# Performance work log

Hardware: AMD Instinct MI355X
Metric: run time of the kernel (lower is better)

## Reference

```python
import jax, jax.numpy as jnp
import numpy as np

TEMPERATURE = 0.1
WEIGHT = 0.1
EPS = 1e-12  # F.normalize clamp_min eps

B = 512   # number of reactions (batches)
G = 128   # atoms per reaction per side (uniform groups)
D = 256   # feature dim


def setup_inputs() -> dict:
    key = jax.random.key(0)
    k1, k2, k3, k4 = jax.random.split(key, 4)
    preds = jax.random.normal(k1, (B,), dtype=jnp.float32)
    y = jax.random.normal(k2, (B,), dtype=jnp.float32)
    reactant_features = jax.random.normal(k3, (B * G, D), dtype=jnp.float32)
    product_features = jax.random.normal(k4, (B * G, D), dtype=jnp.float32)
    # sorted, uniform-size groups: [0]*G, [1]*G, ...
    batch_idx = jnp.repeat(jnp.arange(B, dtype=jnp.int64), G)
    return {
        "preds": preds,
        "y": y,
        "reactant_features": reactant_features,
        "product_features": product_features,
        "reactant_batch_indices": batch_idx,
        "product_batch_indices": batch_idx,
    }


def _l2_normalize(x):
    # matches F.normalize(p=2, dim=1): x / max(||x||, eps)
    n = jnp.sqrt(jnp.sum(x * x, axis=-1, keepdims=True))
    return x / jnp.maximum(n, EPS)


def reference(preds, y, reactant_features, product_features,
              reactant_batch_indices, product_batch_indices):
    # MSE with reduction='sum'
    mse_loss = jnp.sum((preds - y) ** 2)

    # groups are uniform and sorted -> per-batch gather == reshape
    nb = int(reactant_batch_indices[-1]) + 1          # number of unique batches
    g = reactant_features.shape[0] // nb
    d = reactant_features.shape[1]
    r = reactant_features.reshape(nb, g, d)
    p = product_features.reshape(nb, g, d)

    rn = _l2_normalize(r)
    pn = _l2_normalize(p)
    # per-batch similarity [nb, g, g]
    sim = jnp.einsum('bgd,bhd->bgh', rn, pn) / TEMPERATURE

    # cross_entropy with labels = arange(g), mean over rows (torch default)
    lse = jax.scipy.special.logsumexp(sim, axis=-1)   # [nb, g]
    diag = jnp.einsum('bgg->bg', sim)                 # logits at true labels
    ce_per_batch = jnp.mean(lse - diag, axis=-1)      # [nb]
    contrastive_loss = jnp.mean(ce_per_batch)         # sum over batches / nb

    return mse_loss + WEIGHT * contrastive_loss
```

## Files before the change

kernel.cpp:

```cpp
#include <hip/hip_runtime.h>
#include <hip/hip_bf16.h>
#include <math.h>

#define BATCH 512
#define G 128
#define D 256
#define LRP 264

typedef __attribute__((ext_vector_type(8))) short short8;
typedef __attribute__((ext_vector_type(4))) float f32x4;
typedef __attribute__((ext_vector_type(4))) int  i32x4;

__device__ __forceinline__ unsigned short bfbits(float x) {
    __hip_bfloat16 h = __float2bfloat16(x);
    union { __hip_bfloat16 h; unsigned short u; } c; c.h = h; return c.u;
}
__device__ __forceinline__ unsigned int pack2bf16(float a, float b) {
    return (unsigned int)bfbits(a) | ((unsigned int)bfbits(b) << 16);
}

__global__ __launch_bounds__(512, 4)
void fused_kernel(const float* __restrict__ rfeat,
                  const float* __restrict__ pfeat,
                  const float* __restrict__ preds,
                  const float* __restrict__ yv,
                  float* __restrict__ out)
{
    const int b = blockIdx.x;
    const float* rb = rfeat + (size_t)b * (G * D);
    const float* pb = pfeat + (size_t)b * (G * D);

    __shared__ unsigned short ps[64 * LRP];
    __shared__ float inv_r[G];
    __shared__ float inv_p[G];
    __shared__ float red[8];

    const int tid  = threadIdx.x;
    const int lane = tid & 63;
    const int wv   = tid >> 6;
    const int lg   = lane >> 4;
    const int lc   = lane & 15;

    const int srow = tid >> 4;
    const int sc4  = tid & 15;

    float contrib = 0.f;
    if (b == 0) {
        float dd = preds[tid] - yv[tid];
        contrib = dd * dd;
    }

    short8 afr[8];
    float nrsum = 0.f;
    const float* rptr = rb + (wv * 16 + lc) * D + lg * 8;
#pragma unroll
    for (int ks = 0; ks < 8; ++ks) {
        float4 x0 = *reinterpret_cast<const float4*>(rptr + ks * 32);
        float4 x1 = *reinterpret_cast<const float4*>(rptr + ks * 32 + 4);
        nrsum += x0.x*x0.x + x0.y*x0.y + x0.z*x0.z + x0.w*x0.w
               + x1.x*x1.x + x1.y*x1.y + x1.z*x1.z + x1.w*x1.w;
        i32x4 pk = { (int)pack2bf16(x0.x, x0.y), (int)pack2bf16(x0.z, x0.w),
                     (int)pack2bf16(x1.x, x1.y), (int)pack2bf16(x1.z, x1.w) };
        union { i32x4 i; short8 s; } u; u.i = pk;
        afr[ks] = u.s;
    }
    nrsum += __shfl_xor(nrsum, 16);
    nrsum += __shfl_xor(nrsum, 32);
    if (lane < 16)
        inv_r[wv * 16 + lane] = 10.0f / fmaxf(sqrtf(nrsum), 1e-12f);

    float4 pv[2][4];
#pragma unroll
    for (int it = 0; it < 2; ++it)
#pragma unroll
        for (int j = 0; j < 4; ++j)
            pv[it][j] = *reinterpret_cast<const float4*>(pb + (srow + 32 * it) * D + (sc4 + 16 * j) * 4);
#pragma unroll
    for (int it = 0; it < 2; ++it) {
        const int row = srow + 32 * it;
        float s = 0.f;
#pragma unroll
        for (int j = 0; j < 4; ++j) {
            const float4 v = pv[it][j];
            s += v.x*v.x + v.y*v.y + v.z*v.z + v.w*v.w;
            *reinterpret_cast<uint2*>(&ps[row * LRP + (sc4 + 16 * j) * 4]) =
                make_uint2(pack2bf16(v.x, v.y), pack2bf16(v.z, v.w));
        }
#pragma unroll
        for (int off = 1; off < 16; off <<= 1) s += __shfl_xor(s, off);
        if (sc4 == 0) inv_p[row] = 1.0f / fmaxf(sqrtf(s), 1e-12f);
    }
    __syncthreads();

    float4 qv[2][4];
#pragma unroll
    for (int it = 0; it < 2; ++it)
#pragma unroll
        for (int j = 0; j < 4; ++j)
            qv[it][j] = *reinterpret_cast<const float4*>(pb + (64 + srow + 32 * it) * D + (sc4 + 16 * j) * 4);

    f32x4 acc[8];
#pragma unroll
    for (int nj = 0; nj < 8; ++nj) acc[nj] = (f32x4){0.f, 0.f, 0.f, 0.f};

#pragma unroll
    for (int ks = 0; ks < 8; ++ks) {
        const int kb = ks * 32 + lg * 8;
#pragma unroll
        for (int nj = 0; nj < 4; ++nj) {
            short8 bfr = *reinterpret_cast<const short8*>(&ps[(nj * 16 + lc) * LRP + kb]);
            acc[nj] = __builtin_amdgcn_mfma_f32_16x16x32_bf16(afr[ks], bfr, acc[nj], 0, 0, 0);
        }
    }
    __syncthreads();

#pragma unroll
    for (int it = 0; it < 2; ++it) {
        const int row = srow + 32 * it;
        float s = 0.f;
#pragma unroll
        for (int j = 0; j < 4; ++j) {
            const float4 v = qv[it][j];
            s += v.x*v.x + v.y*v.y + v.z*v.z + v.w*v.w;
            *reinterpret_cast<uint2*>(&ps[row * LRP + (sc4 + 16 * j) * 4]) =
                make_uint2(pack2bf16(v.x, v.y), pack2bf16(v.z, v.w));
        }
#pragma unroll
        for (int off = 1; off < 16; off <<= 1) s += __shfl_xor(s, off);
        if (sc4 == 0) inv_p[64 + row] = 1.0f / fmaxf(sqrtf(s), 1e-12f);
    }
    __syncthreads();

#pragma unroll
    for (int ks = 0; ks < 8; ++ks) {
        const int kb = ks * 32 + lg * 8;
#pragma unroll
        for (int nj = 0; nj < 4; ++nj) {
            short8 bfr = *reinterpret_cast<const short8*>(&ps[(nj * 16 + lc) * LRP + kb]);
            acc[4 + nj] = __builtin_amdgcn_mfma_f32_16x16x32_bf16(afr[ks], bfr, acc[4 + nj], 0, 0, 0);
        }
    }

    float invp_r[8];
#pragma unroll
    for (int nj = 0; nj < 8; ++nj) invp_r[nj] = inv_p[nj * 16 + lc];

    const int njd = wv;
    float ce_part = 0.f;
#pragma unroll
    for (int reg = 0; reg < 4; ++reg) {
        const int rrow = lg * 4 + reg;
        const float invr_g = inv_r[wv * 16 + rrow];
        float s[8];
        float m = -3.0e38f;
#pragma unroll
        for (int nj = 0; nj < 8; ++nj) {
            s[nj] = acc[nj][reg] * invr_g * invp_r[nj];
            m = fmaxf(m, s[nj]);
        }
#pragma unroll
        for (int off = 1; off < 16; off <<= 1) m = fmaxf(m, __shfl_xor(m, off));
        float e = 0.f;
#pragma unroll
        for (int nj = 0; nj < 8; ++nj) e += __expf(s[nj] - m);
#pragma unroll
        for (int off = 1; off < 16; off <<= 1) e += __shfl_xor(e, off);
        if (lc == rrow)
            ce_part += (m + __logf(e)) - s[njd];
    }

    contrib += ce_part * (0.1f / ((float)BATCH * (float)G));
#pragma unroll
    for (int off = 1; off < 64; off <<= 1) contrib += __shfl_xor(contrib, off);
    if (lane == 0) red[wv] = contrib;
    __syncthreads();
    if (tid == 0) {
        float t = 0.f;
#pragma unroll
        for (int i = 0; i < 8; ++i) t += red[i];
        atomicAdd(out, t);
    }
}

extern "C" void kernel_launch(void* const* d_in, const int* in_sizes, int n_in,
                              void* d_out, int out_size, void* d_ws, size_t ws_size,
                              hipStream_t stream) {
    const float* preds = (const float*)d_in[0];
    const float* yv    = (const float*)d_in[1];
    const float* rf    = (const float*)d_in[2];
    const float* pf    = (const float*)d_in[3];
    float* out = (float*)d_out;
    (void)d_ws; (void)ws_size;

    hipMemsetAsync(out, 0, (size_t)out_size * sizeof(float), stream);
    fused_kernel<<<BATCH, 512, 0, stream>>>(rf, pf, preds, yv, out);
}
```

Measured before the change: 35.91 us.

## Split each row group's column tiles across two waves with 1024-thread blocks

Doubles the block to 16 waves. Each pair of waves shares a 16-row group of reactants and each wave computes half of the 128 product columns. Per-row max and exp-sum partials go through shared memory and are merged with a log-sum-exp combine. The goal is more waves in flight to hide global-load latency and cut MFMA work per wave. In exchange, each reactant row is loaded twice and the kernel adds an extra barrier, shared-memory traffic and a launch bound of 1024 threads that may limit registers.

```diff
diff --git a/kernel.cpp b/kernel.cpp
--- a/kernel.cpp
+++ b/kernel.cpp
@@ -19,7 +19,7 @@
     return (unsigned int)bfbits(a) | ((unsigned int)bfbits(b) << 16);
 }
 
-__global__ __launch_bounds__(512, 4)
+__global__ __launch_bounds__(1024, 8)
 void fused_kernel(const float* __restrict__ rfeat,
                   const float* __restrict__ pfeat,
                   const float* __restrict__ preds,
@@ -33,26 +33,30 @@
     __shared__ unsigned short ps[64 * LRP];
     __shared__ float inv_r[G];
     __shared__ float inv_p[G];
-    __shared__ float red[8];
+    __shared__ float smm[G][2];
+    __shared__ float sme[G][2];
+    __shared__ float red[16];
 
     const int tid  = threadIdx.x;
     const int lane = tid & 63;
     const int wv   = tid >> 6;
+    const int rg   = wv >> 1;
+    const int ch   = wv & 1;
     const int lg   = lane >> 4;
     const int lc   = lane & 15;
 
-    const int srow = tid >> 4;
+    const int prow = tid >> 4;
     const int sc4  = tid & 15;
 
     float contrib = 0.f;
-    if (b == 0) {
+    if (b == 0 && tid < 512) {
         float dd = preds[tid] - yv[tid];
         contrib = dd * dd;
     }
 
     short8 afr[8];
     float nrsum = 0.f;
-    const float* rptr = rb + (wv * 16 + lc) * D + lg * 8;
+    const float* rptr = rb + (rg * 16 + lc) * D + lg * 8;
 #pragma unroll
     for (int ks = 0; ks < 8; ++ks) {
         float4 x0 = *reinterpret_cast<const float4*>(rptr + ks * 32);
@@ -67,67 +71,59 @@
     nrsum += __shfl_xor(nrsum, 16);
     nrsum += __shfl_xor(nrsum, 32);
     if (lane < 16)
-        inv_r[wv * 16 + lane] = 10.0f / fmaxf(sqrtf(nrsum), 1e-12f);
-
-    float4 pv[2][4];
-#pragma unroll
-    for (int it = 0; it < 2; ++it)
-#pragma unroll
-        for (int j = 0; j < 4; ++j)
-            pv[it][j] = *reinterpret_cast<const float4*>(pb + (srow + 32 * it) * D + (sc4 + 16 * j) * 4);
-#pragma unroll
-    for (int it = 0; it < 2; ++it) {
-        const int row = srow + 32 * it;
-        float s = 0.f;
+        inv_r[rg * 16 + lane] = 10.0f / fmaxf(sqrtf(nrsum), 1e-12f);
+
+    float4 pv[4];
+#pragma unroll
+    for (int j = 0; j < 4; ++j)
+        pv[j] = *reinterpret_cast<const float4*>(pb + prow * D + (sc4 + 16 * j) * 4);
+    {
+        float ss = 0.f;
 #pragma unroll
         for (int j = 0; j < 4; ++j) {
-            const float4 v = pv[it][j];
-            s += v.x*v.x + v.y*v.y + v.z*v.z + v.w*v.w;
-            *reinterpret_cast<uint2*>(&ps[row * LRP + (sc4 + 16 * j) * 4]) =
+            const float4 v = pv[j];
+            ss += v.x*v.x + v.y*v.y + v.z*v.z + v.w*v.w;
+            *reinterpret_cast<uint2*>(&ps[prow * LRP + (sc4 + 16 * j) * 4]) =
                 make_uint2(pack2bf16(v.x, v.y), pack2bf16(v.z, v.w));
         }
 #pragma unroll
-        for (int off = 1; off < 16; off <<= 1) s += __shfl_xor(s, off);
-        if (sc4 == 0) inv_p[row] = 1.0f / fmaxf(sqrtf(s), 1e-12f);
-    }
-    __syncthreads();
-
-    float4 qv[2][4];
-#pragma unroll
-    for (int it = 0; it < 2; ++it)
-#pragma unroll
-        for (int j = 0; j < 4; ++j)
-            qv[it][j] = *reinterpret_cast<const float4*>(pb + (64 + srow + 32 * it) * D + (sc4 + 16 * j) * 4);
-
-    f32x4 acc[8];
-#pragma unroll
-    for (int nj = 0; nj < 8; ++nj) acc[nj] = (f32x4){0.f, 0.f, 0.f, 0.f};
+        for (int off = 1; off < 16; off <<= 1) ss += __shfl_xor(ss, off);
+        if (sc4 == 0) inv_p[prow] = 1.0f / fmaxf(sqrtf(ss), 1e-12f);
+    }
+    __syncthreads();
+
+    float4 qv[4];
+#pragma unroll
+    for (int j = 0; j < 4; ++j)
+        qv[j] = *reinterpret_cast<const float4*>(pb + (64 + prow) * D + (sc4 + 16 * j) * 4);
+
+    f32x4 acc[4];
+#pragma unroll
+    for (int i = 0; i < 4; ++i) acc[i] = (f32x4){0.f, 0.f, 0.f, 0.f};
 
 #pragma unroll
     for (int ks = 0; ks < 8; ++ks) {
         const int kb = ks * 32 + lg * 8;
 #pragma unroll
-        for (int nj = 0; nj < 4; ++nj) {
-            short8 bfr = *reinterpret_cast<const short8*>(&ps[(nj * 16 + lc) * LRP + kb]);
-            acc[nj] = __builtin_amdgcn_mfma_f32_16x16x32_bf16(afr[ks], bfr, acc[nj], 0, 0, 0);
-        }
-    }
-    __syncthreads();
-
-#pragma unroll
-    for (int it = 0; it < 2; ++it) {
-        const int row = srow + 32 * it;
-        float s = 0.f;
+        for (int i = 0; i < 2; ++i) {
+            short8 bfr = *reinterpret_cast<const short8*>(&ps[((2 * ch + i) * 16 + lc) * LRP + kb]);
+            acc[i] = __builtin_amdgcn_mfma_f32_16x16x32_bf16(afr[ks], bfr, acc[i], 0, 0, 0);
+        }
+    }
+    __syncthreads();
+
+    {
+        float ss = 0.f;
 #pragma unroll
         for (int j = 0; j < 4; ++j) {
-            const float4 v = qv[it][j];
-            s += v.x*v.x + v.y*v.y + v.z*v.z + v.w*v.w;
-            *reinterpret_cast<uint2*>(&ps[row * LRP + (sc4 + 16 * j) * 4]) =
+            const float4 v = qv[j];
+            ss += v.x*v.x + v.y*v.y + v.z*v.z + v.w*v.w;
+            *reinterpret_cast<uint2*>(&ps[prow * LRP + (sc4 + 16 * j) * 4]) =
                 make_uint2(pack2bf16(v.x, v.y), pack2bf16(v.z, v.w));
         }
 #pragma unroll
-        for (int off = 1; off < 16; off <<= 1) s += __shfl_xor(s, off);
-        if (sc4 == 0) inv_p[64 + row] = 1.0f / fmaxf(sqrtf(s), 1e-12f);
+        for (int off = 1; off < 16; off <<= 1) ss += __shfl_xor(ss, off);
+        if (sc4 == 0) inv_p[64 + prow] = 1.0f / fmaxf(sqrtf(ss), 1e-12f);
     }
     __syncthreads();
 
@@ -135,38 +131,62 @@
     for (int ks = 0; ks < 8; ++ks) {
         const int kb = ks * 32 + lg * 8;
 #pragma unroll
-        for (int nj = 0; nj < 4; ++nj) {
-            short8 bfr = *reinterpret_cast<const short8*>(&ps[(nj * 16 + lc) * LRP + kb]);
-            acc[4 + nj] = __builtin_amdgcn_mfma_f32_16x16x32_bf16(afr[ks], bfr, acc[4 + nj], 0, 0, 0);
-        }
-    }
-
-    float invp_r[8];
-#pragma unroll
-    for (int nj = 0; nj < 8; ++nj) invp_r[nj] = inv_p[nj * 16 + lc];
-
-    const int njd = wv;
-    float ce_part = 0.f;
+        for (int i = 0; i < 2; ++i) {
+            short8 bfr = *reinterpret_cast<const short8*>(&ps[((2 * ch + i) * 16 + lc) * LRP + kb]);
+            acc[2 + i] = __builtin_amdgcn_mfma_f32_16x16x32_bf16(afr[ks], bfr, acc[2 + i], 0, 0, 0);
+        }
+    }
+
+    float invp_w[4];
+    invp_w[0] = inv_p[(2 * ch)     * 16 + lc];
+    invp_w[1] = inv_p[(2 * ch + 1) * 16 + lc];
+    invp_w[2] = inv_p[(4 + 2 * ch) * 16 + lc];
+    invp_w[3] = inv_p[(5 + 2 * ch) * 16 + lc];
+
+    const int chd = (rg >> 1) & 1;
+    const int idg = (rg & 1) + 2 * (rg >> 2);
+    float sdiag[4];
+
 #pragma unroll
     for (int reg = 0; reg < 4; ++reg) {
         const int rrow = lg * 4 + reg;
-        const float invr_g = inv_r[wv * 16 + rrow];
-        float s[8];
+        const float invr_g = inv_r[rg * 16 + rrow];
+        float s[4];
         float m = -3.0e38f;
 #pragma unroll
-        for (int nj = 0; nj < 8; ++nj) {
-            s[nj] = acc[nj][reg] * invr_g * invp_r[nj];
-            m = fmaxf(m, s[nj]);
+        for (int i = 0; i < 4; ++i) {
+            s[i] = acc[i][reg] * invr_g * invp_w[i];
+            m = fmaxf(m, s[i]);
         }
 #pragma unroll
         for (int off = 1; off < 16; off <<= 1) m = fmaxf(m, __shfl_xor(m, off));
         float e = 0.f;
 #pragma unroll
-        for (int nj = 0; nj < 8; ++nj) e += __expf(s[nj] - m);
+        for (int i = 0; i < 4; ++i) e += __expf(s[i] - m);
 #pragma unroll
         for (int off = 1; off < 16; off <<= 1) e += __shfl_xor(e, off);
-        if (lc == rrow)
-            ce_part += (m + __logf(e)) - s[njd];
+        if (lc == 0) {
+            smm[rg * 16 + rrow][ch] = m;
+            sme[rg * 16 + rrow][ch] = e;
+        }
+        sdiag[reg] = s[idg];
+    }
+    __syncthreads();
+
+    float ce_part = 0.f;
+    if (ch == chd) {
+#pragma unroll
+        for (int reg = 0; reg < 4; ++reg) {
+            const int rrow = lg * 4 + reg;
+            if (lc == rrow) {
+                const int grow = rg * 16 + rrow;
+                float m0 = smm[grow][0], m1 = smm[grow][1];
+                float e0 = sme[grow][0], e1 = sme[grow][1];
+                float mm = fmaxf(m0, m1);
+                float E  = e0 * __expf(m0 - mm) + e1 * __expf(m1 - mm);
+                ce_part += mm + __logf(E) - sdiag[reg];
+            }
+        }
     }
 
     contrib += ce_part * (0.1f / ((float)BATCH * (float)G));
@@ -177,7 +197,7 @@
     if (tid == 0) {
         float t = 0.f;
 #pragma unroll
-        for (int i = 0; i < 8; ++i) t += red[i];
+        for (int i = 0; i < 16; ++i) t += red[i];
         atomicAdd(out, t);
     }
 }
@@ -193,5 +213,5 @@
     (void)d_ws; (void)ws_size;
 
     hipMemsetAsync(out, 0, (size_t)out_size * sizeof(float), stream);
-    fused_kernel<<<BATCH, 512, 0, stream>>>(rf, pf, preds, yv, out);
-}
+    fused_kernel<<<BATCH, 1024, 0, stream>>>(rf, pf, preds, yv, out);
+}
```

Result: slower. 81.77 us (+127.7%).
